# Kernel tuning notes

Measured on AMD Instinct MI355X. Metric: run time of the kernel, lower is better.

Reference implementation:

```python
import jax, jax.numpy as jnp
from jax import lax
import numpy as np

NEG_INF = -1000000000.0  # matches torch masked_fill value
POS_THRESH = -100000000.0


def setup_inputs() -> dict:
    key = jax.random.key(0)
    k1, k2, k3 = jax.random.split(key, 3)
    B, C_in, L = 1, 16, 2048
    C_out, groups, K = 16, 4, 3
    scores = jax.random.normal(k1, (B, C_in, L, L), dtype=jnp.float32)
    weight = jax.random.normal(k2, (C_out, C_in // groups, K, K), dtype=jnp.float32) * 0.1
    bias = jax.random.normal(k3, (C_out,), dtype=jnp.float32) * 0.1
    return {"scores": scores, "weight": weight, "bias": bias}


def reference(scores, weight, bias):
    B, C_in, L, _ = scores.shape
    C_out, cpg, K, _ = weight.shape
    groups = C_in // cpg
    mask = jnp.tril(jnp.ones((L, L), dtype=bool))[None, None]  # (1,1,L,L) causal

    s = scores.astype(jnp.float32)
    z = jnp.where(mask, s, NEG_INF)

    # sparsemax over last axis: sort desc, cumsum, support-size threshold
    z_sorted = -jnp.sort(-z, axis=-1)                 # descending
    cum_sum = jnp.cumsum(z_sorted, axis=-1)
    k_idx = jnp.arange(1, L + 1, dtype=z.dtype)        # (L,) broadcasts over (B,C,L,L)
    cond = (1.0 + k_idx * z_sorted > cum_sum) & (z_sorted > POS_THRESH)
    k_sp = jnp.sum(cond, axis=-1, keepdims=True)       # support size, int
    k_safe = jnp.maximum(k_sp, 1)
    cum_sum_k = jnp.take_along_axis(cum_sum, k_safe - 1, axis=-1)
    tau = (cum_sum_k - 1.0) / k_safe.astype(z.dtype)
    tau = jnp.where(k_sp == 0, jnp.inf, tau)
    probs = jnp.maximum(z - tau, 0.0)                  # (B,C_in,L,L)

    # grouped same-padded conv2d over the (L,L) score map
    out = lax.conv_general_dilated(
        probs, weight,
        window_strides=(1, 1),
        padding=[(K // 2, K // 2), (K // 2, K // 2)],
        feature_group_count=groups,
        dimension_numbers=("NCHW", "OIHW", "NCHW"),
    )
    out = out + bias[None, :, None, None]
    out = jnp.where(mask, out, 0.0)
    return out.astype(scores.dtype)
```

## Files before the change

### kernel.cpp

```cpp
#include <hip/hip_runtime.h>

#define L 2048
#define CIN 16
#define GROUPS 4
#define NEG_INF -1000000000.0f

__global__ __launch_bounds__(256) void tau_kernel(const float* __restrict__ scores,
                                                  float* __restrict__ tau_out) {
    const int wid  = (blockIdx.x << 2) + (threadIdx.x >> 6);
    const int lane = threadIdx.x & 63;
    const int ch   = wid >> 11;
    const int row  = wid & 2047;
    const int n    = row + 1;
    const float* zrow = scores + ((size_t)ch * L + row) * L;

    float v[32];
    float m = NEG_INF;
#pragma unroll
    for (int j = 0; j < 8; ++j) {
        int c4 = lane + (j << 6);
        int c  = c4 << 2;
        float4 z = make_float4(NEG_INF, NEG_INF, NEG_INF, NEG_INF);
        if (c < n) z = *((const float4*)zrow + c4);
        v[4*j+0] = (c + 0 < n) ? z.x : NEG_INF;
        v[4*j+1] = (c + 1 < n) ? z.y : NEG_INF;
        v[4*j+2] = (c + 2 < n) ? z.z : NEG_INF;
        v[4*j+3] = (c + 3 < n) ? z.w : NEG_INF;
        m = fmaxf(m, fmaxf(fmaxf(v[4*j+0], v[4*j+1]), fmaxf(v[4*j+2], v[4*j+3])));
    }
#pragma unroll
    for (int d = 32; d; d >>= 1) m = fmaxf(m, __shfl_xor(m, d, 64));

    float tau = m - 1.0f;
    int k_prev = -1;
    for (int it = 0; it < 64; ++it) {
        float S = 0.0f, Kf = 0.0f;
#pragma unroll
        for (int j = 0; j < 32; ++j) {
            if (v[j] > tau) { S += v[j]; Kf += 1.0f; }
        }
#pragma unroll
        for (int d = 32; d; d >>= 1) {
            S  += __shfl_xor(S,  d, 64);
            Kf += __shfl_xor(Kf, d, 64);
        }
        int K = (int)Kf;
        if (K == k_prev) break;
        tau = (S - 1.0f) / Kf;
        k_prev = K;
    }
    if (lane == 0) tau_out[ch * L + row] = tau;
}

#define TR 16
#define TC 64
#define HR 18
#define HCS 68

__global__ __launch_bounds__(256) void conv_kernel(const float* __restrict__ scores,
                                                   const float* __restrict__ tau,
                                                   const float* __restrict__ weight,
                                                   const float* __restrict__ bias,
                                                   float* __restrict__ out) {
    const int c0 = blockIdx.x * TC;
    const int r0 = blockIdx.y * TR;
    const int g  = blockIdx.z;
    const int t  = threadIdx.x;

    if (c0 > r0 + TR - 1) {
#pragma unroll
        for (int jj = 0; jj < 4; ++jj) {
            int idx = t + jj * 256;
            int c4  = idx & 15;
            int r   = (idx >> 4) & 15;
            int o   = idx >> 8;
            float4* p = (float4*)(out + (((size_t)(g * 4 + o) * L + (r0 + r)) * L + c0)) + c4;
            *p = make_float4(0.f, 0.f, 0.f, 0.f);
        }
        return;
    }

    __shared__ __align__(16) float P[4][HR][HCS];

    for (int i = 0; i < 4; ++i) {
        const float* srcbase = scores + (size_t)(g * 4 + i) * L * L;
        const float* taubase = tau + (g * 4 + i) * L;
#pragma unroll
        for (int rnd = 0; rnd < 2; ++rnd) {
            int idx = t + rnd * 256;
            if (idx < HR * 16) {
                int hr = idx >> 4;
                int c4 = idx & 15;
                int r  = r0 - 1 + hr;
                int cb = c0 + (c4 << 2);
                float4 val = make_float4(0.f, 0.f, 0.f, 0.f);
                if (r >= 0 && r < L && cb <= r) {
                    float tv = taubase[r];
                    float4 z = *((const float4*)(srcbase + (size_t)r * L) + (cb >> 2));
                    val.x = fmaxf(z.x - tv, 0.f);
                    val.y = (cb + 1 <= r) ? fmaxf(z.y - tv, 0.f) : 0.f;
                    val.z = (cb + 2 <= r) ? fmaxf(z.z - tv, 0.f) : 0.f;
                    val.w = (cb + 3 <= r) ? fmaxf(z.w - tv, 0.f) : 0.f;
                }
                *((float4*)&P[i][hr][c4 << 2]) = val;
            }
        }
    }
    if (t < 144) {
        int side = t & 1;
        int j  = t >> 1;
        int i  = j / 18;
        int hr = j - i * 18;
        int r  = r0 - 1 + hr;
        int c  = side ? (c0 + TC) : (c0 - 1);
        float val = 0.f;
        if (r >= 0 && r < L && c >= 0 && c <= r) {
            val = fmaxf(scores[((size_t)(g * 4 + i) * L + r) * L + c]
                        - tau[(g * 4 + i) * L + r], 0.f);
        }
        P[i][hr][64 + side] = val;
    }
    __syncthreads();

    const int o   = __builtin_amdgcn_readfirstlane(t >> 6);
    const int col = t & 63;
    const int cg  = c0 + col;

    float w[4][9];
#pragma unroll
    for (int i = 0; i < 4; ++i)
#pragma unroll
        for (int k = 0; k < 9; ++k) w[i][k] = weight[((g * 4 + o) * 4 + i) * 9 + k];
    const float b = bias[g * 4 + o];

    const int xl = (col == 0)  ? 64 : col - 1;
    const int xm = col;
    const int xr = (col == 63) ? 65 : col + 1;

    float win[4][3][3];
#pragma unroll
    for (int i = 0; i < 4; ++i) {
        win[i][1][0] = P[i][0][xl]; win[i][1][1] = P[i][0][xm]; win[i][1][2] = P[i][0][xr];
        win[i][2][0] = P[i][1][xl]; win[i][2][1] = P[i][1][xm]; win[i][2][2] = P[i][1][xr];
    }

    const size_t outbase = ((size_t)(g * 4 + o) * L + r0) * L + cg;
#pragma unroll
    for (int rr = 0; rr < TR; ++rr) {
#pragma unroll
        for (int i = 0; i < 4; ++i) {
#pragma unroll
            for (int dx = 0; dx < 3; ++dx) {
                win[i][0][dx] = win[i][1][dx];
                win[i][1][dx] = win[i][2][dx];
            }
            win[i][2][0] = P[i][rr + 2][xl];
            win[i][2][1] = P[i][rr + 2][xm];
            win[i][2][2] = P[i][rr + 2][xr];
        }
        float acc = b;
#pragma unroll
        for (int i = 0; i < 4; ++i)
#pragma unroll
            for (int dy = 0; dy < 3; ++dy)
#pragma unroll
                for (int dx = 0; dx < 3; ++dx)
                    acc = fmaf(win[i][dy][dx], w[i][3 * dy + dx], acc);
        out[outbase + (size_t)rr * L] = (cg <= r0 + rr) ? acc : 0.0f;
    }
}

extern "C" void kernel_launch(void* const* d_in, const int* in_sizes, int n_in,
                              void* d_out, int out_size, void* d_ws, size_t ws_size,
                              hipStream_t stream) {
    const float* scores = (const float*)d_in[0];
    const float* weight = (const float*)d_in[1];
    const float* bias   = (const float*)d_in[2];
    float* out = (float*)d_out;
    float* tau = (float*)d_ws;

    tau_kernel<<<(CIN * L) / 4, 256, 0, stream>>>(scores, tau);

    dim3 gridB(L / TC, L / TR, GROUPS);
    conv_kernel<<<gridB, 256, 0, stream>>>(scores, tau, weight, bias, out);
}
```

Baseline: 534.0 us.

## Replace shared-memory conv tile with register sliding window and lane shuffles

The conv kernel no longer stages a halo tile in LDS. Each wave now covers 256 columns, with each lane computing 4 output columns as a float4. Rows are streamed into a 3-row register window and horizontal neighbours are exchanged with wave shuffles, which drops the __syncthreads and LDS traffic and makes stores vectorised. In exchange, each wave (one per output channel) reloads the same input rows from global/L2, so input reads are duplicated 4x within a block, and the wider tiles coarsen the skipping of masked blocks.

Measured after the change: 797.0 us. +49.3%, slower.

```diff
diff --git a/kernel.cpp b/kernel.cpp
--- a/kernel.cpp
+++ b/kernel.cpp
@@ -53,120 +53,110 @@
 }
 
 #define TR 16
-#define TC 64
-#define HR 18
-#define HCS 68
+#define TCW 256
+
+struct Row6 { float4 v; float lw, rx; };
 
 __global__ __launch_bounds__(256) void conv_kernel(const float* __restrict__ scores,
                                                    const float* __restrict__ tau,
                                                    const float* __restrict__ weight,
                                                    const float* __restrict__ bias,
                                                    float* __restrict__ out) {
-    const int c0 = blockIdx.x * TC;
-    const int r0 = blockIdx.y * TR;
-    const int g  = blockIdx.z;
-    const int t  = threadIdx.x;
+    const int c0   = blockIdx.x * TCW;
+    const int r0   = blockIdx.y * TR;
+    const int g    = blockIdx.z;
+    const int t    = threadIdx.x;
+    const int o    = __builtin_amdgcn_readfirstlane(t >> 6);
+    const int lane = t & 63;
+    const int go   = g * 4 + o;
+    const int c    = c0 + (lane << 2);
+    float* outp = out + ((size_t)go * L + r0) * L + c;
 
     if (c0 > r0 + TR - 1) {
+        const float4 z4 = make_float4(0.f, 0.f, 0.f, 0.f);
 #pragma unroll
-        for (int jj = 0; jj < 4; ++jj) {
-            int idx = t + jj * 256;
-            int c4  = idx & 15;
-            int r   = (idx >> 4) & 15;
-            int o   = idx >> 8;
-            float4* p = (float4*)(out + (((size_t)(g * 4 + o) * L + (r0 + r)) * L + c0)) + c4;
-            *p = make_float4(0.f, 0.f, 0.f, 0.f);
-        }
+        for (int rr = 0; rr < TR; ++rr)
+            *(float4*)(outp + (size_t)rr * L) = z4;
         return;
     }
-
-    __shared__ __align__(16) float P[4][HR][HCS];
-
-    for (int i = 0; i < 4; ++i) {
-        const float* srcbase = scores + (size_t)(g * 4 + i) * L * L;
-        const float* taubase = tau + (g * 4 + i) * L;
-#pragma unroll
-        for (int rnd = 0; rnd < 2; ++rnd) {
-            int idx = t + rnd * 256;
-            if (idx < HR * 16) {
-                int hr = idx >> 4;
-                int c4 = idx & 15;
-                int r  = r0 - 1 + hr;
-                int cb = c0 + (c4 << 2);
-                float4 val = make_float4(0.f, 0.f, 0.f, 0.f);
-                if (r >= 0 && r < L && cb <= r) {
-                    float tv = taubase[r];
-                    float4 z = *((const float4*)(srcbase + (size_t)r * L) + (cb >> 2));
-                    val.x = fmaxf(z.x - tv, 0.f);
-                    val.y = (cb + 1 <= r) ? fmaxf(z.y - tv, 0.f) : 0.f;
-                    val.z = (cb + 2 <= r) ? fmaxf(z.z - tv, 0.f) : 0.f;
-                    val.w = (cb + 3 <= r) ? fmaxf(z.w - tv, 0.f) : 0.f;
-                }
-                *((float4*)&P[i][hr][c4 << 2]) = val;
-            }
-        }
-    }
-    if (t < 144) {
-        int side = t & 1;
-        int j  = t >> 1;
-        int i  = j / 18;
-        int hr = j - i * 18;
-        int r  = r0 - 1 + hr;
-        int c  = side ? (c0 + TC) : (c0 - 1);
-        float val = 0.f;
-        if (r >= 0 && r < L && c >= 0 && c <= r) {
-            val = fmaxf(scores[((size_t)(g * 4 + i) * L + r) * L + c]
-                        - tau[(g * 4 + i) * L + r], 0.f);
-        }
-        P[i][hr][64 + side] = val;
-    }
-    __syncthreads();
-
-    const int o   = __builtin_amdgcn_readfirstlane(t >> 6);
-    const int col = t & 63;
-    const int cg  = c0 + col;
 
     float w[4][9];
 #pragma unroll
     for (int i = 0; i < 4; ++i)
 #pragma unroll
-        for (int k = 0; k < 9; ++k) w[i][k] = weight[((g * 4 + o) * 4 + i) * 9 + k];
-    const float b = bias[g * 4 + o];
+        for (int k = 0; k < 9; ++k) w[i][k] = weight[(go * 4 + i) * 9 + k];
+    const float b = bias[go];
 
-    const int xl = (col == 0)  ? 64 : col - 1;
-    const int xm = col;
-    const int xr = (col == 63) ? 65 : col + 1;
+    auto load_row = [&](int i, int r) -> Row6 {
+        Row6 R;
+        float4 z = make_float4(0.f, 0.f, 0.f, 0.f);
+        float ev = 0.f;
+        if (r >= 0 && r < L) {
+            const float tv = tau[(g * 4 + i) * L + r];
+            const float* srow = scores + ((size_t)(g * 4 + i) * L + r) * L;
+            if (c <= r) {
+                float4 zz = *(const float4*)(srow + c);
+                z.x = fmaxf(zz.x - tv, 0.f);
+                z.y = (c + 1 <= r) ? fmaxf(zz.y - tv, 0.f) : 0.f;
+                z.z = (c + 2 <= r) ? fmaxf(zz.z - tv, 0.f) : 0.f;
+                z.w = (c + 3 <= r) ? fmaxf(zz.w - tv, 0.f) : 0.f;
+            }
+            const int ec = (lane == 0) ? (c0 - 1) : (c0 + TCW);
+            if ((lane == 0 || lane == 63) && ec >= 0 && ec <= r)
+                ev = fmaxf(srow[ec] - tv, 0.f);
+        }
+        float lw = __shfl_up(z.w, 1, 64);
+        float rx = __shfl_down(z.x, 1, 64);
+        R.v  = z;
+        R.lw = (lane == 0)  ? ev : lw;
+        R.rx = (lane == 63) ? ev : rx;
+        return R;
+    };
 
-    float win[4][3][3];
+    Row6 win[4][3];
 #pragma unroll
     for (int i = 0; i < 4; ++i) {
-        win[i][1][0] = P[i][0][xl]; win[i][1][1] = P[i][0][xm]; win[i][1][2] = P[i][0][xr];
-        win[i][2][0] = P[i][1][xl]; win[i][2][1] = P[i][1][xm]; win[i][2][2] = P[i][1][xr];
+        win[i][0] = load_row(i, r0 - 1);
+        win[i][1] = load_row(i, r0);
     }
 
-    const size_t outbase = ((size_t)(g * 4 + o) * L + r0) * L + cg;
 #pragma unroll
     for (int rr = 0; rr < TR; ++rr) {
 #pragma unroll
+        for (int i = 0; i < 4; ++i)
+            win[i][(rr + 2) % 3] = load_row(i, r0 + rr + 1);
+
+        float4 acc = make_float4(b, b, b, b);
+#pragma unroll
         for (int i = 0; i < 4; ++i) {
 #pragma unroll
-            for (int dx = 0; dx < 3; ++dx) {
-                win[i][0][dx] = win[i][1][dx];
-                win[i][1][dx] = win[i][2][dx];
+            for (int dy = 0; dy < 3; ++dy) {
+                const Row6& R = win[i][(rr + dy) % 3];
+                const float w0 = w[i][dy * 3 + 0];
+                const float w1 = w[i][dy * 3 + 1];
+                const float w2 = w[i][dy * 3 + 2];
+                acc.x = fmaf(R.lw,  w0, acc.x);
+                acc.x = fmaf(R.v.x, w1, acc.x);
+                acc.x = fmaf(R.v.y, w2, acc.x);
+                acc.y = fmaf(R.v.x, w0, acc.y);
+                acc.y = fmaf(R.v.y, w1, acc.y);
+                acc.y = fmaf(R.v.z, w2, acc.y);
+                acc.z = fmaf(R.v.y, w0, acc.z);
+                acc.z = fmaf(R.v.z, w1, acc.z);
+                acc.z = fmaf(R.v.w, w2, acc.z);
+                acc.w = fmaf(R.v.z, w0, acc.w);
+                acc.w = fmaf(R.v.w, w1, acc.w);
+                acc.w = fmaf(R.rx,  w2, acc.w);
             }
-            win[i][2][0] = P[i][rr + 2][xl];
-            win[i][2][1] = P[i][rr + 2][xm];
-            win[i][2][2] = P[i][rr + 2][xr];
         }
-        float acc = b;
-#pragma unroll
-        for (int i = 0; i < 4; ++i)
-#pragma unroll
-            for (int dy = 0; dy < 3; ++dy)
-#pragma unroll
-                for (int dx = 0; dx < 3; ++dx)
-                    acc = fmaf(win[i][dy][dx], w[i][3 * dy + dx], acc);
-        out[outbase + (size_t)rr * L] = (cg <= r0 + rr) ? acc : 0.0f;
+
+        const int r = r0 + rr;
+        float4 res;
+        res.x = (c     <= r) ? acc.x : 0.f;
+        res.y = (c + 1 <= r) ? acc.y : 0.f;
+        res.z = (c + 2 <= r) ? acc.z : 0.f;
+        res.w = (c + 3 <= r) ? acc.w : 0.f;
+        *(float4*)(outp + (size_t)rr * L) = res;
     }
 }
 
@@ -181,6 +171,6 @@
 
     tau_kernel<<<(CIN * L) / 4, 256, 0, stream>>>(scores, tau);
 
-    dim3 gridB(L / TC, L / TR, GROUPS);
+    dim3 gridB(L / TCW, L / TR, GROUPS);
     conv_kernel<<<gridB, 256, 0, stream>>>(scores, tau, weight, bias, out);
 }
```

## Sort-based sparsemax tau via ballot compaction; wider conv tiles with float4 register blocking

Applied to the files above, without the earlier changes.

The tau kernel ballot-compacts the candidates above max-1 into shared memory. When there are at most 64 of them it finds the threshold with one wave-wide bitonic sort and prefix scan, instead of the iterative fixed-point loop. The conv kernel widens the tile to 128 columns, and each thread computes 4 columns by 8 rows using float4 loads from shared memory, a sliding row window and vectorised stores. Interior tiles get a separate fast path with no causal-mask checks. This cuts the per-row iteration cost and the shared-memory reads per output, at the cost of more registers and a __syncthreads in the tau kernel.

After: 531.2 us. About the same (-0.5%).

```diff
diff --git a/kernel.cpp b/kernel.cpp
--- a/kernel.cpp
+++ b/kernel.cpp
@@ -3,12 +3,14 @@
 #define L 2048
 #define CIN 16
 #define GROUPS 4
-#define NEG_INF -1000000000.0f
+#define NEG_INF  -1000000000.0f
+#define POS_THRESH -100000000.0f
 
 __global__ __launch_bounds__(256) void tau_kernel(const float* __restrict__ scores,
                                                   float* __restrict__ tau_out) {
     const int wid  = (blockIdx.x << 2) + (threadIdx.x >> 6);
     const int lane = threadIdx.x & 63;
+    const int ws   = threadIdx.x >> 6;
     const int ch   = wid >> 11;
     const int row  = wid & 2047;
     const int n    = row + 1;
@@ -31,142 +33,249 @@
 #pragma unroll
     for (int d = 32; d; d >>= 1) m = fmaxf(m, __shfl_xor(m, d, 64));
 
-    float tau = m - 1.0f;
-    int k_prev = -1;
-    for (int it = 0; it < 64; ++it) {
-        float S = 0.0f, Kf = 0.0f;
-#pragma unroll
-        for (int j = 0; j < 32; ++j) {
-            if (v[j] > tau) { S += v[j]; Kf += 1.0f; }
-        }
-#pragma unroll
-        for (int d = 32; d; d >>= 1) {
-            S  += __shfl_xor(S,  d, 64);
-            Kf += __shfl_xor(Kf, d, 64);
-        }
-        int K = (int)Kf;
-        if (K == k_prev) break;
-        tau = (S - 1.0f) / Kf;
-        k_prev = K;
+    const float thr = m - 1.0f;
+
+    __shared__ float buf[4][64];
+    int base = 0;
+#pragma unroll
+    for (int j = 0; j < 32; ++j) {
+        bool p = v[j] > thr;
+        unsigned long long mask = __ballot(p);
+        if (mask) {
+            if (p) {
+                int pos = __builtin_amdgcn_mbcnt_lo((unsigned)mask, 0);
+                pos = __builtin_amdgcn_mbcnt_hi((unsigned)(mask >> 32), pos);
+                pos += base;
+                if (pos < 64) buf[ws][pos] = v[j];
+            }
+            base += __popcll(mask);
+        }
+    }
+    __syncthreads();
+    const int cnt = base;
+
+    float tau;
+    if (cnt <= 64) {
+        float x = (lane < cnt) ? buf[ws][lane] : NEG_INF;
+#pragma unroll
+        for (int k = 2; k <= 64; k <<= 1) {
+#pragma unroll
+            for (int j = k >> 1; j > 0; j >>= 1) {
+                float p = __shfl_xor(x, j, 64);
+                bool desc    = ((lane & k) == 0);
+                bool earlier = ((lane & j) == 0);
+                float mx = fmaxf(x, p), mn = fminf(x, p);
+                x = (desc == earlier) ? mx : mn;
+            }
+        }
+        float csum = x;
+#pragma unroll
+        for (int d = 1; d < 64; d <<= 1) {
+            float y = __shfl_up(csum, d, 64);
+            if (lane >= d) csum += y;
+        }
+        bool cond = (1.0f + (float)(lane + 1) * x > csum) && (x > POS_THRESH);
+        unsigned long long cmask = __ballot(cond);
+        int k = (int)__popcll(cmask);
+        float ck = __shfl(csum, k - 1, 64);
+        tau = (ck - 1.0f) / (float)k;
+    } else {
+        tau = thr;
+        int k_prev = -1;
+        for (int it = 0; it < 64; ++it) {
+            float S = 0.0f, Kf = 0.0f;
+#pragma unroll
+            for (int j = 0; j < 32; ++j)
+                if (v[j] > tau) { S += v[j]; Kf += 1.0f; }
+#pragma unroll
+            for (int d = 32; d; d >>= 1) {
+                S  += __shfl_xor(S,  d, 64);
+                Kf += __shfl_xor(Kf, d, 64);
+            }
+            int K = (int)Kf;
+            if (K == k_prev) break;
+            tau = (S - 1.0f) / Kf;
+            k_prev = K;
+        }
     }
     if (lane == 0) tau_out[ch * L + row] = tau;
 }
 
 #define TR 16
-#define TC 64
+#define TC 128
 #define HR 18
-#define HCS 68
-
-__global__ __launch_bounds__(256) void conv_kernel(const float* __restrict__ scores,
-                                                   const float* __restrict__ tau,
-                                                   const float* __restrict__ weight,
-                                                   const float* __restrict__ bias,
-                                                   float* __restrict__ out) {
+#define PST 132
+
+struct W6 { float l, m0, m1, m2, m3, r; };
+
+__global__ __launch_bounds__(256, 4) void conv_kernel(const float* __restrict__ scores,
+                                                      const float* __restrict__ tau,
+                                                      const float* __restrict__ weight,
+                                                      const float* __restrict__ bias,
+                                                      float* __restrict__ out) {
     const int c0 = blockIdx.x * TC;
     const int r0 = blockIdx.y * TR;
     const int g  = blockIdx.z;
     const int t  = threadIdx.x;
 
     if (c0 > r0 + TR - 1) {
-#pragma unroll
-        for (int jj = 0; jj < 4; ++jj) {
-            int idx = t + jj * 256;
-            int c4  = idx & 15;
-            int r   = (idx >> 4) & 15;
-            int o   = idx >> 8;
-            float4* p = (float4*)(out + (((size_t)(g * 4 + o) * L + (r0 + r)) * L + c0)) + c4;
-            *p = make_float4(0.f, 0.f, 0.f, 0.f);
+        const float4 z4 = make_float4(0.f, 0.f, 0.f, 0.f);
+#pragma unroll
+        for (int jj = 0; jj < 8; ++jj) {
+            int idx = t + (jj << 8);
+            int c4  = idx & 31;
+            int r   = (idx >> 5) & 15;
+            int o   = idx >> 9;
+            float4* p = (float4*)(out + (((size_t)((g << 2) + o) * L + (r0 + r)) * L + c0)) + c4;
+            *p = z4;
         }
         return;
     }
 
-    __shared__ __align__(16) float P[4][HR][HCS];
-
-    for (int i = 0; i < 4; ++i) {
-        const float* srcbase = scores + (size_t)(g * 4 + i) * L * L;
-        const float* taubase = tau + (g * 4 + i) * L;
-#pragma unroll
-        for (int rnd = 0; rnd < 2; ++rnd) {
-            int idx = t + rnd * 256;
-            if (idx < HR * 16) {
-                int hr = idx >> 4;
-                int c4 = idx & 15;
-                int r  = r0 - 1 + hr;
-                int cb = c0 + (c4 << 2);
-                float4 val = make_float4(0.f, 0.f, 0.f, 0.f);
-                if (r >= 0 && r < L && cb <= r) {
-                    float tv = taubase[r];
-                    float4 z = *((const float4*)(srcbase + (size_t)r * L) + (cb >> 2));
+    __shared__ __align__(16) float P[4][HR][PST];
+
+    const bool interior = (c0 >= 1) && (c0 + TC + 1 <= r0) && (r0 + TR <= L - 1);
+
+    if (interior) {
+        for (int ic = 0; ic < 4; ++ic) {
+            const float* sb = scores + (size_t)((g << 2) + ic) * L * L;
+            const float* tb = tau + ((g << 2) + ic) * L;
+#pragma unroll
+            for (int kk = 0; kk < 3; ++kk) {
+                int idx = t + (kk << 8);
+                if (idx < HR * 32) {
+                    int hr = idx >> 5;
+                    int c4 = idx & 31;
+                    int r  = r0 - 1 + hr;
+                    float tv = tb[r];
+                    float4 z = *((const float4*)(sb + (size_t)r * L + c0) + c4);
+                    float4 val;
                     val.x = fmaxf(z.x - tv, 0.f);
-                    val.y = (cb + 1 <= r) ? fmaxf(z.y - tv, 0.f) : 0.f;
-                    val.z = (cb + 2 <= r) ? fmaxf(z.z - tv, 0.f) : 0.f;
-                    val.w = (cb + 3 <= r) ? fmaxf(z.w - tv, 0.f) : 0.f;
+                    val.y = fmaxf(z.y - tv, 0.f);
+                    val.z = fmaxf(z.z - tv, 0.f);
+                    val.w = fmaxf(z.w - tv, 0.f);
+                    *((float4*)&P[ic][hr][c4 << 2]) = val;
                 }
-                *((float4*)&P[i][hr][c4 << 2]) = val;
-            }
-        }
-    }
-    if (t < 144) {
-        int side = t & 1;
-        int j  = t >> 1;
-        int i  = j / 18;
-        int hr = j - i * 18;
-        int r  = r0 - 1 + hr;
-        int c  = side ? (c0 + TC) : (c0 - 1);
-        float val = 0.f;
-        if (r >= 0 && r < L && c >= 0 && c <= r) {
-            val = fmaxf(scores[((size_t)(g * 4 + i) * L + r) * L + c]
-                        - tau[(g * 4 + i) * L + r], 0.f);
-        }
-        P[i][hr][64 + side] = val;
+            }
+        }
+        if (t < 144) {
+            int side = t & 1, j = t >> 1;
+            int ic = j / HR, hr = j - ic * HR;
+            int r = r0 - 1 + hr;
+            int c = side ? (c0 + TC) : (c0 - 1);
+            float tv = tau[((g << 2) + ic) * L + r];
+            float z  = scores[((size_t)((g << 2) + ic) * L + r) * L + c];
+            P[ic][hr][side ? TC : 131] = fmaxf(z - tv, 0.f);
+        }
+    } else {
+        for (int ic = 0; ic < 4; ++ic) {
+            const float* sb = scores + (size_t)((g << 2) + ic) * L * L;
+            const float* tb = tau + ((g << 2) + ic) * L;
+#pragma unroll
+            for (int kk = 0; kk < 3; ++kk) {
+                int idx = t + (kk << 8);
+                if (idx < HR * 32) {
+                    int hr = idx >> 5;
+                    int c4 = idx & 31;
+                    int r  = r0 - 1 + hr;
+                    int cb = c0 + (c4 << 2);
+                    float4 val = make_float4(0.f, 0.f, 0.f, 0.f);
+                    if (r >= 0 && r < L && cb <= r) {
+                        float tv = tb[r];
+                        float4 z = *((const float4*)(sb + (size_t)r * L) + (cb >> 2));
+                        val.x = fmaxf(z.x - tv, 0.f);
+                        val.y = (cb + 1 <= r) ? fmaxf(z.y - tv, 0.f) : 0.f;
+                        val.z = (cb + 2 <= r) ? fmaxf(z.z - tv, 0.f) : 0.f;
+                        val.w = (cb + 3 <= r) ? fmaxf(z.w - tv, 0.f) : 0.f;
+                    }
+                    *((float4*)&P[ic][hr][c4 << 2]) = val;
+                }
+            }
+        }
+        if (t < 144) {
+            int side = t & 1, j = t >> 1;
+            int ic = j / HR, hr = j - ic * HR;
+            int r = r0 - 1 + hr;
+            int c = side ? (c0 + TC) : (c0 - 1);
+            float val = 0.f;
+            if (r >= 0 && r < L && c >= 0 && c <= r) {
+                val = fmaxf(scores[((size_t)((g << 2) + ic) * L + r) * L + c]
+                            - tau[((g << 2) + ic) * L + r], 0.f);
+            }
+            P[ic][hr][side ? TC : 131] = val;
+        }
     }
     __syncthreads();
 
-    const int o   = __builtin_amdgcn_readfirstlane(t >> 6);
-    const int col = t & 63;
-    const int cg  = c0 + col;
+    const int o    = __builtin_amdgcn_readfirstlane(t >> 6);
+    const int lane = t & 63;
+    const int col4 = lane & 31;
+    const int rh   = lane >> 5;
+    const int hb   = rh << 3;
+    const int go   = (g << 2) + o;
+    const int cb   = c0 + (col4 << 2);
+    const int li   = col4 ? ((col4 << 2) - 2) : 130;
+    const int ri   = (col4 << 2) + 4;
 
     float w[4][9];
 #pragma unroll
-    for (int i = 0; i < 4; ++i)
-#pragma unroll
-        for (int k = 0; k < 9; ++k) w[i][k] = weight[((g * 4 + o) * 4 + i) * 9 + k];
-    const float b = bias[g * 4 + o];
-
-    const int xl = (col == 0)  ? 64 : col - 1;
-    const int xm = col;
-    const int xr = (col == 63) ? 65 : col + 1;
-
-    float win[4][3][3];
-#pragma unroll
-    for (int i = 0; i < 4; ++i) {
-        win[i][1][0] = P[i][0][xl]; win[i][1][1] = P[i][0][xm]; win[i][1][2] = P[i][0][xr];
-        win[i][2][0] = P[i][1][xl]; win[i][2][1] = P[i][1][xm]; win[i][2][2] = P[i][1][xr];
-    }
-
-    const size_t outbase = ((size_t)(g * 4 + o) * L + r0) * L + cg;
-#pragma unroll
-    for (int rr = 0; rr < TR; ++rr) {
-#pragma unroll
-        for (int i = 0; i < 4; ++i) {
-#pragma unroll
-            for (int dx = 0; dx < 3; ++dx) {
-                win[i][0][dx] = win[i][1][dx];
-                win[i][1][dx] = win[i][2][dx];
-            }
-            win[i][2][0] = P[i][rr + 2][xl];
-            win[i][2][1] = P[i][rr + 2][xm];
-            win[i][2][2] = P[i][rr + 2][xr];
-        }
-        float acc = b;
-#pragma unroll
-        for (int i = 0; i < 4; ++i)
-#pragma unroll
-            for (int dy = 0; dy < 3; ++dy)
-#pragma unroll
-                for (int dx = 0; dx < 3; ++dx)
-                    acc = fmaf(win[i][dy][dx], w[i][3 * dy + dx], acc);
-        out[outbase + (size_t)rr * L] = (cg <= r0 + rr) ? acc : 0.0f;
+    for (int ic = 0; ic < 4; ++ic)
+#pragma unroll
+        for (int k = 0; k < 9; ++k) w[ic][k] = weight[((go << 2) + ic) * 9 + k];
+    const float bb = bias[go];
+
+    auto ldwin = [&](int ic, int hr) -> W6 {
+        const float* rp = &P[ic][hr][0];
+        float4 M  = *(const float4*)(rp + (col4 << 2));
+        float2 Lv = *(const float2*)(rp + li);
+        float2 Rv = *(const float2*)(rp + ri);
+        W6 q; q.l = Lv.y; q.m0 = M.x; q.m1 = M.y; q.m2 = M.z; q.m3 = M.w; q.r = Rv.x;
+        return q;
+    };
+
+    float4 acc[8];
+#pragma unroll
+    for (int rr = 0; rr < 8; ++rr) acc[rr] = make_float4(bb, bb, bb, bb);
+
+#pragma unroll
+    for (int ic = 0; ic < 4; ++ic) {
+        W6 a = ldwin(ic, hb);
+        W6 b = ldwin(ic, hb + 1);
+#pragma unroll
+        for (int rr = 0; rr < 8; ++rr) {
+            W6 c = ldwin(ic, hb + rr + 2);
+            const W6 rows[3] = { a, b, c };
+#pragma unroll
+            for (int dy = 0; dy < 3; ++dy) {
+                const W6& q = rows[dy];
+                const float w0 = w[ic][dy * 3 + 0];
+                const float w1 = w[ic][dy * 3 + 1];
+                const float w2 = w[ic][dy * 3 + 2];
+                acc[rr].x = fmaf(q.l,  w0, fmaf(q.m0, w1, fmaf(q.m1, w2, acc[rr].x)));
+                acc[rr].y = fmaf(q.m0, w0, fmaf(q.m1, w1, fmaf(q.m2, w2, acc[rr].y)));
+                acc[rr].z = fmaf(q.m1, w0, fmaf(q.m2, w1, fmaf(q.m3, w2, acc[rr].z)));
+                acc[rr].w = fmaf(q.m2, w0, fmaf(q.m3, w1, fmaf(q.r,  w2, acc[rr].w)));
+            }
+            a = b; b = c;
+        }
+    }
+
+    float* outp = out + ((size_t)go * L + (r0 + hb)) * L + cb;
+    if (interior) {
+#pragma unroll
+        for (int rr = 0; rr < 8; ++rr)
+            *(float4*)(outp + (size_t)rr * L) = acc[rr];
+    } else {
+#pragma unroll
+        for (int rr = 0; rr < 8; ++rr) {
+            int r = r0 + hb + rr;
+            float4 res;
+            res.x = (cb     <= r) ? acc[rr].x : 0.f;
+            res.y = (cb + 1 <= r) ? acc[rr].y : 0.f;
+            res.z = (cb + 2 <= r) ? acc[rr].z : 0.f;
+            res.w = (cb + 3 <= r) ? acc[rr].w : 0.f;
+            *(float4*)(outp + (size_t)rr * L) = res;
+        }
     }
 }
 
```
